# Kernel optimization log

Hardware: AMD Instinct MI355X
Metric: run time of the kernel (lower is better)

## Reference

```python
import jax, jax.numpy as jnp
import numpy as np

B, T, M, PH, PW = 4, 8, 128, 48, 48
QD, CD, H, DH = 1024, 768, 8, 64
INNER = H * DH

def layer_norm(x, g, b, eps=1e-5):
    m = x.mean(-1, keepdims=True)
    v = ((x - m) ** 2).mean(-1, keepdims=True)
    return (x - m) * jax.lax.rsqrt(v + eps) * g + b

def setup_inputs():
    key = jax.random.key(0)
    ks = jax.random.split(key, 10)
    x = jax.random.normal(ks[0], (B * T, PH * PW, QD), jnp.float32)
    context = jax.random.normal(ks[1], (B, M, CD), jnp.float32)
    sg_node_positions = jax.random.normal(ks[2], (B, M, 3), jnp.float32) * 2.0
    # valid c2w: identity rotation + random translation (invertible)
    c2w = jnp.broadcast_to(jnp.eye(4, dtype=jnp.float32), (B, T, 4, 4))
    camera_c2w = c2w.at[..., :3, 3].set(jax.random.normal(ks[3], (B, T, 3), jnp.float32))
    intrinsics = jnp.broadcast_to(jnp.array([[1.0, 0.0, 0.5], [0.0, 1.0, 0.5], [0.0, 0.0, 1.0]], jnp.float32), (B, 3, 3))
    s = 0.02
    Wq = jax.random.normal(ks[4], (QD, INNER), jnp.float32) * s
    Wk = jax.random.normal(ks[5], (CD, INNER), jnp.float32) * s
    Wv = jax.random.normal(ks[6], (CD, INNER), jnp.float32) * s
    Wo = jax.random.normal(ks[7], (INNER, QD), jnp.float32) * s
    gate = jnp.array([0.1], jnp.float32)          # zero-init in module; nonzero so path is active
    spatial_gate = jnp.array([0.1], jnp.float32)
    spatial_log_sigma = jax.random.normal(ks[8], (H,), jnp.float32) * 0.1
    depth_log_alpha = jax.random.normal(ks[9], (H,), jnp.float32) * 0.1
    gamma_q = jnp.ones((QD,), jnp.float32); beta_q = jnp.zeros((QD,), jnp.float32)
    gamma_k = jnp.ones((CD,), jnp.float32); beta_k = jnp.zeros((CD,), jnp.float32)
    return dict(x=x, context=context, sg_node_positions=sg_node_positions, camera_c2w=camera_c2w,
                intrinsics=intrinsics, Wq=Wq, Wk=Wk, Wv=Wv, Wo=Wo, gate=gate, spatial_gate=spatial_gate,
                spatial_log_sigma=spatial_log_sigma, depth_log_alpha=depth_log_alpha,
                gamma_q=gamma_q, beta_q=beta_q, gamma_k=gamma_k, beta_k=beta_k,
                patch_h=PH, patch_w=PW)

def spatial_bias(sg_node_positions, camera_c2w, intrinsics, spatial_log_sigma, depth_log_alpha, patch_h, patch_w):
    Bb, Mn, _ = sg_node_positions.shape
    Tn = camera_c2w.shape[1]
    w2c = jnp.linalg.inv(camera_c2w)
    R = w2c[:, :, :3, :3]
    tv = w2c[:, :, :3, 3]
    p_cam = jnp.einsum('btij,bmj->btmi', R, sg_node_positions) + tv[:, :, None, :]  # (B,T,M,3)
    z = jnp.clip(p_cam[..., 2], 1e-4, None)
    fx = intrinsics[:, 0, 0]; fy = intrinsics[:, 1, 1]
    cx = intrinsics[:, 0, 2]; cy = intrinsics[:, 1, 2]
    u = fx[:, None, None] * (p_cam[..., 0] / z) + cx[:, None, None]   # (B,T,M)
    v = fy[:, None, None] * (p_cam[..., 1] / z) + cy[:, None, None]
    gy = (jnp.arange(patch_h, dtype=jnp.float32) + 0.5) / patch_h
    gx = (jnp.arange(patch_w, dtype=jnp.float32) + 0.5) / patch_w
    gyy, gxx = jnp.meshgrid(gy, gx, indexing='ij')
    gxx = gxx.reshape(-1); gyy = gyy.reshape(-1)                       # (P,)
    sq = (gxx[None, None, :, None] - u[:, :, None, :]) ** 2 + (gyy[None, None, :, None] - v[:, :, None, :]) ** 2  # (B,T,P,M)
    sigma = jnp.exp(spatial_log_sigma)
    inv2s = z[:, :, None, :] ** 2 / (2.0 * sigma[None, None, :, None] ** 2 + 1e-8)  # (B,T,H,M)
    bias = -sq[:, :, None, :, :] * inv2s[:, :, :, None, :]             # (B,T,H,P,M)
    depth_term = depth_log_alpha[None, None, :, None, None] * (-jnp.log(z))[:, :, None, None, :]
    bias = bias + depth_term
    behind = p_cam[..., 2] <= 0.0
    bias = jnp.where(behind[:, :, None, None, :], 0.0, bias)
    return bias.reshape(Bb * Tn, bias.shape[2], patch_h * patch_w, Mn)  # (BT,H,P,M)

def reference(x, context, sg_node_positions, camera_c2w, intrinsics, Wq, Wk, Wv, Wo, gate, spatial_gate,
              spatial_log_sigma, depth_log_alpha, gamma_q, beta_q, gamma_k, beta_k, patch_h, patch_w):
    BT, P, _ = x.shape
    Bb, Mn, _ = context.shape
    Tn = camera_c2w.shape[1]
    q = layer_norm(x, gamma_q, beta_q) @ Wq                            # (BT,P,INNER)
    ck = layer_norm(context, gamma_k, beta_k)
    k = ck @ Wk
    v = ck @ Wv
    q = q.reshape(BT, P, H, DH).transpose(0, 2, 1, 3)                  # (BT,H,P,DH)
    k = jnp.broadcast_to(k.reshape(Bb, 1, Mn, H, DH), (Bb, Tn, Mn, H, DH)).reshape(BT, Mn, H, DH).transpose(0, 2, 1, 3)
    v = jnp.broadcast_to(v.reshape(Bb, 1, Mn, H, DH), (Bb, Tn, Mn, H, DH)).reshape(BT, Mn, H, DH).transpose(0, 2, 1, 3)
    scores = jnp.einsum('bhpd,bhmd->bhpm', q, k) * (DH ** -0.5)        # (BT,H,P,M)
    bias = spatial_bias(sg_node_positions, camera_c2w, intrinsics, spatial_log_sigma, depth_log_alpha, patch_h, patch_w)
    scores = scores + jnp.tanh(spatial_gate) * bias
    attn = jax.nn.softmax(scores, axis=-1)
    out = jnp.einsum('bhpm,bhmd->bhpd', attn, v).transpose(0, 2, 1, 3).reshape(BT, P, INNER)
    return x + jnp.tanh(gate) * (out @ Wo)
```

## Files before the change

kernel.cpp:

```cpp
#include <hip/hip_runtime.h>
#include <hip/hip_bf16.h>
#include <stdint.h>
#include <cstddef>

typedef short short8 __attribute__((ext_vector_type(8)));
typedef float f32x4 __attribute__((ext_vector_type(4)));
typedef unsigned short us4 __attribute__((ext_vector_type(4)));
typedef unsigned short us8 __attribute__((ext_vector_type(8)));

#define DEV static __device__ __forceinline__

DEV unsigned short f2b(float f) {
  __hip_bfloat16 h = __float2bfloat16(f);
  return __builtin_bit_cast(unsigned short, h);
}
DEV float b2f(unsigned short u) {
  unsigned int t = ((unsigned int)u) << 16;
  return __builtin_bit_cast(float, t);
}

DEV void gload_lds16(const void* g, void* lds) {
  __builtin_amdgcn_global_load_lds((const __attribute__((address_space(1))) unsigned int*)g,
                                   (__attribute__((address_space(3))) unsigned int*)lds, 16, 0, 0);
}

__launch_bounds__(512, 2)
__global__ void gemm256_8ph(const unsigned short* __restrict__ A,
                            const unsigned short* __restrict__ Bt,
                            unsigned short* __restrict__ Cb,
                            int M, int N, int K)
{
  __shared__ __attribute__((aligned(16))) char lds[131072];
  const int tid = threadIdx.x;
  const int lane = tid & 63, w = tid >> 6;
  const int wr = w >> 2, wc = w & 3;
  const int g = lane >> 4, lr = lane & 15;
  const int ntile = N >> 8;
  const int nwg = gridDim.x;
  const int bid = blockIdx.x;
  const int tile = ((nwg & 7) == 0) ? ((bid & 7)*(nwg >> 3) + (bid >> 3)) : bid;
  const size_t m0 = (size_t)(tile / ntile) << 8;
  const size_t n0 = (size_t)(tile % ntile) << 8;

  const int srl = tid >> 3;
  const int sgc = ((tid & 7) ^ (srl & 7)) * 8;

#define STAGEH(X, grow0, k0, ldsoff)                                           \
  do {                                                                         \
    char* hb_ = lds + (ldsoff) + w*1024;                                       \
    gload_lds16((X) + ((grow0) + srl)*(size_t)K + (k0) + sgc, hb_);            \
    gload_lds16((X) + ((grow0) + 64 + srl)*(size_t)K + (k0) + sgc, hb_ + 8192);\
  } while (0)

#define BAR() do { __builtin_amdgcn_sched_barrier(0); __builtin_amdgcn_s_barrier(); __builtin_amdgcn_sched_barrier(0); } while (0)

  f32x4 acc[8][4] = {};
  short8 aF[4][2], bF[4][2];

  int aoff[2], boff[2];
#pragma unroll
  for (int kk = 0; kk < 2; ++kk) {
    const int sl = (((kk*4 + g) ^ (lr & 7)) * 16);
    aoff[kk] = wr*16384 + lr*128 + sl;
    boff[kk] = 32768 + (wc >> 1)*16384 + ((wc & 1)*64 + lr)*128 + sl;
  }

#define MFQ(mh, nh)                                                            \
  do {                                                                         \
    __builtin_amdgcn_s_setprio(1);                                             \
    _Pragma("unroll")                                                          \
    for (int kk = 0; kk < 2; ++kk)                                             \
      _Pragma("unroll")                                                        \
      for (int mt = 0; mt < 4; ++mt)                                           \
        _Pragma("unroll")                                                      \
        for (int nt = 0; nt < 2; ++nt)                                         \
          acc[(mh)*4+mt][(nh)*2+nt] = __builtin_amdgcn_mfma_f32_16x16x32_bf16( \
              aF[mt][kk], bF[(nh)*2+nt][kk], acc[(mh)*4+mt][(nh)*2+nt], 0,0,0);\
    __builtin_amdgcn_s_setprio(0);                                             \
  } while (0)

  STAGEH(A,  m0,       0, 0);
  STAGEH(A,  m0 + 128, 0, 16384);
  STAGEH(Bt, n0,       0, 32768);
  STAGEH(Bt, n0 + 128, 0, 49152);
  STAGEH(Bt, n0,       64, 65536 + 32768);
  STAGEH(Bt, n0 + 128, 64, 65536 + 49152);
  asm volatile("s_waitcnt vmcnt(4)" ::: "memory");
  __builtin_amdgcn_s_barrier();

  const int NI = K >> 7;
  for (int i = 0; i < NI; ++i) {
    const int T = 2*i;
    const bool nl = (i + 1 < NI);
    const int kA1 = (T + 1) << 6;
    const int kT2 = (T + 2) << 6;
    const int kT3 = (T + 3) << 6;

#pragma unroll
    for (int kk = 0; kk < 2; ++kk) {
#pragma unroll
      for (int mt = 0; mt < 4; ++mt) aF[mt][kk] = *(const short8*)(lds + mt*2048 + aoff[kk]);
#pragma unroll
      for (int nf = 0; nf < 2; ++nf) bF[nf][kk] = *(const short8*)(lds + nf*2048 + boff[kk]);
    }
    STAGEH(A, m0, kA1, 65536);
    BAR();
    MFQ(0, 0);
    BAR();
#pragma unroll
    for (int kk = 0; kk < 2; ++kk)
#pragma unroll
      for (int nf = 2; nf < 4; ++nf) bF[nf][kk] = *(const short8*)(lds + nf*2048 + boff[kk]);
    STAGEH(A, m0 + 128, kA1, 65536 + 16384);
    BAR();
    MFQ(0, 1);
    BAR();
#pragma unroll
    for (int kk = 0; kk < 2; ++kk)
#pragma unroll
      for (int mt = 0; mt < 4; ++mt) aF[mt][kk] = *(const short8*)(lds + (4+mt)*2048 + aoff[kk]);
    if (nl) STAGEH(Bt, n0, kT2, 32768);
    BAR();
    MFQ(1, 0);
    BAR();
    if (nl) {
      STAGEH(Bt, n0 + 128, kT2, 49152);
      asm volatile("s_waitcnt vmcnt(4)" ::: "memory");
    } else {
      asm volatile("s_waitcnt vmcnt(0)" ::: "memory");
    }
    BAR();
    MFQ(1, 1);
    BAR();

#pragma unroll
    for (int kk = 0; kk < 2; ++kk) {
#pragma unroll
      for (int mt = 0; mt < 4; ++mt) aF[mt][kk] = *(const short8*)(lds + 65536 + mt*2048 + aoff[kk]);
#pragma unroll
      for (int nf = 0; nf < 2; ++nf) bF[nf][kk] = *(const short8*)(lds + 65536 + nf*2048 + boff[kk]);
    }
    if (nl) STAGEH(A, m0, kT2, 0);
    BAR();
    MFQ(0, 0);
    BAR();
#pragma unroll
    for (int kk = 0; kk < 2; ++kk)
#pragma unroll
      for (int nf = 2; nf < 4; ++nf) bF[nf][kk] = *(const short8*)(lds + 65536 + nf*2048 + boff[kk]);
    if (nl) STAGEH(A, m0 + 128, kT2, 16384);
    BAR();
    MFQ(0, 1);
    BAR();
#pragma unroll
    for (int kk = 0; kk < 2; ++kk)
#pragma unroll
      for (int mt = 0; mt < 4; ++mt) aF[mt][kk] = *(const short8*)(lds + 65536 + (4+mt)*2048 + aoff[kk]);
    if (nl) STAGEH(Bt, n0, kT3, 65536 + 32768);
    BAR();
    MFQ(1, 0);
    BAR();
    if (nl) {
      STAGEH(Bt, n0 + 128, kT3, 65536 + 49152);
      asm volatile("s_waitcnt vmcnt(4)" ::: "memory");
    }
    BAR();
    MFQ(1, 1);
    BAR();
  }

  asm volatile("s_waitcnt vmcnt(0)" ::: "memory");
  __builtin_amdgcn_s_barrier();
  float* Sw = (float*)(lds) + w*1024;
#pragma unroll
  for (int mt = 0; mt < 8; ++mt) {
#pragma unroll
    for (int nt = 0; nt < 4; ++nt)
#pragma unroll
      for (int r = 0; r < 4; ++r)
        Sw[(g*4 + r)*64 + nt*16 + lr] = acc[mt][nt][r];
#pragma unroll
    for (int rep = 0; rep < 2; ++rep) {
      const int row2 = rep*8 + (lane >> 3);
      const int colf = (lane & 7)*8;
      f32x4 a0 = *(const f32x4*)(Sw + row2*64 + colf);
      f32x4 a1 = *(const f32x4*)(Sw + row2*64 + colf + 4);
      us8 ov;
#pragma unroll
      for (int j = 0; j < 4; ++j) { ov[j] = f2b(a0[j]); ov[4+j] = f2b(a1[j]); }
      const size_t rowg = m0 + wr*128 + mt*16 + row2;
      *(us8*)(Cb + rowg * (size_t)N + (n0 + wc*64 + colf)) = ov;
    }
  }
#undef STAGEH
#undef BAR
#undef MFQ
}

__launch_bounds__(256, 2)
__global__ void gemm_oproj(const unsigned short* __restrict__ A,
                           const unsigned short* __restrict__ Bt,
                           float* __restrict__ Cf,
                           const unsigned short* __restrict__ lnx,
                           const float* __restrict__ stats,
                           const float* __restrict__ ginv,
                           const float* __restrict__ betaq,
                           const float* __restrict__ gatep,
                           int M, int N, int K)
{
  __shared__ __attribute__((aligned(16))) char As[16384];
  __shared__ __attribute__((aligned(16))) char Bs[16384];
  const int tid  = threadIdx.x;
  const int lane = tid & 63, w = tid >> 6;
  const int wr = w >> 1, wc = w & 1;
  const int g = lane >> 4, lr = lane & 15;
  const int ntile = N >> 7;
  const int nwg = gridDim.x;
  const int bid = blockIdx.x;
  const int tile = ((nwg & 7) == 0) ? ((bid & 7)*(nwg >> 3) + (bid >> 3)) : bid;
  const int m0 = (tile / ntile) << 7;
  const int n0 = (tile % ntile) << 7;

  const int lrow  = lane >> 3;
  const int lslot = (lane & 7) ^ lrow;

  f32x4 acc[4][4] = {};

  for (int k0 = 0; k0 < K; k0 += 64) {
#pragma unroll
    for (int c = 0; c < 4; ++c) {
      const int rowc = (w*4 + c)*8;
      gload_lds16(A  + (size_t)(m0 + rowc + lrow)*K + k0 + lslot*8, As + rowc*128);
      gload_lds16(Bt + (size_t)(n0 + rowc + lrow)*K + k0 + lslot*8, Bs + rowc*128);
    }
    __syncthreads();
#pragma unroll
    for (int ks = 0; ks < 2; ++ks) {
      short8 af[4], bfr[4];
#pragma unroll
      for (int mt = 0; mt < 4; ++mt) {
        int row = wr*64 + mt*16 + lr;
        int slot = (ks*4 + g) ^ (row & 7);
        af[mt] = *(const short8*)(As + row*128 + slot*16);
      }
#pragma unroll
      for (int nt = 0; nt < 4; ++nt) {
        int row = wc*64 + nt*16 + lr;
        int slot = (ks*4 + g) ^ (row & 7);
        bfr[nt] = *(const short8*)(Bs + row*128 + slot*16);
      }
#pragma unroll
      for (int mt = 0; mt < 4; ++mt)
#pragma unroll
        for (int nt = 0; nt < 4; ++nt)
          acc[mt][nt] = __builtin_amdgcn_mfma_f32_16x16x32_bf16(af[mt], bfr[nt], acc[mt][nt], 0, 0, 0);
    }
    __syncthreads();
  }

  float* Sw = (float*)(As) + w*1024;
  const float tg = tanhf(gatep[0]);
#pragma unroll
  for (int mt = 0; mt < 4; ++mt) {
#pragma unroll
    for (int nt = 0; nt < 4; ++nt)
#pragma unroll
      for (int r = 0; r < 4; ++r)
        Sw[(g*4 + r)*64 + nt*16 + lr] = acc[mt][nt][r];
#pragma unroll
    for (int rep = 0; rep < 4; ++rep) {
      const int row2 = rep*4 + g;
      const int colf = lr*4;
      f32x4 val = *(const f32x4*)(Sw + row2*64 + colf);
      const size_t rowg = (size_t)(m0 + wr*64 + mt*16 + row2);
      const size_t col  = (size_t)(n0 + wc*64 + colf);
      const size_t idx  = rowg * (size_t)N + col;
      const float mn = stats[rowg*2 + 0];
      const float sd = stats[rowg*2 + 1];
      us4 lnv = *(const us4*)(lnx + idx);
      f32x4 gi = *(const f32x4*)(ginv + col);
      f32x4 bt4 = *(const f32x4*)(betaq + col);
#pragma unroll
      for (int j = 0; j < 4; ++j) {
        float xr = (b2f(lnv[j]) - bt4[j]) * gi[j] * sd + mn;
        val[j] = xr + tg * val[j];
      }
      *(f32x4*)(Cf + idx) = val;
    }
  }
}

__launch_bounds__(256, 2)
__global__ void gemm_kv(const unsigned short* __restrict__ ck,
                        const unsigned short* __restrict__ Wk_t,
                        const unsigned short* __restrict__ Wv_t,
                        unsigned short* __restrict__ Kb,
                        unsigned short* __restrict__ Vt)
{
  __shared__ __attribute__((aligned(16))) char As[16384];
  __shared__ __attribute__((aligned(16))) char Bs[16384];
  const int bid = blockIdx.x;
  const int kv = bid >> 4, bidl = bid & 15;
  const unsigned short* Bt = kv ? Wv_t : Wk_t;
  const int m0 = (bidl >> 2) << 7, n0 = (bidl & 3) << 7;
  const int tid  = threadIdx.x;
  const int lane = tid & 63, w = tid >> 6;
  const int wr = w >> 1, wc = w & 1;
  const int g = lane >> 4, lr = lane & 15;
  const int lrow  = lane >> 3;
  const int lslot = (lane & 7) ^ lrow;
  const int K = 768;

  f32x4 acc[4][4] = {};

  for (int k0 = 0; k0 < K; k0 += 64) {
#pragma unroll
    for (int c = 0; c < 4; ++c) {
      const int rowc = (w*4 + c)*8;
      gload_lds16(ck + (size_t)(m0 + rowc + lrow)*K + k0 + lslot*8, As + rowc*128);
      gload_lds16(Bt + (size_t)(n0 + rowc + lrow)*K + k0 + lslot*8, Bs + rowc*128);
    }
    __syncthreads();
#pragma unroll
    for (int ks = 0; ks < 2; ++ks) {
      short8 af[4], bfr[4];
#pragma unroll
      for (int mt = 0; mt < 4; ++mt) {
        int row = wr*64 + mt*16 + lr;
        int slot = (ks*4 + g) ^ (row & 7);
        af[mt] = *(const short8*)(As + row*128 + slot*16);
      }
#pragma unroll
      for (int nt = 0; nt < 4; ++nt) {
        int row = wc*64 + nt*16 + lr;
        int slot = (ks*4 + g) ^ (row & 7);
        bfr[nt] = *(const short8*)(Bs + row*128 + slot*16);
      }
#pragma unroll
      for (int mt = 0; mt < 4; ++mt)
#pragma unroll
        for (int nt = 0; nt < 4; ++nt)
          acc[mt][nt] = __builtin_amdgcn_mfma_f32_16x16x32_bf16(af[mt], bfr[nt], acc[mt][nt], 0, 0, 0);
    }
    __syncthreads();
  }

#pragma unroll
  for (int mt = 0; mt < 4; ++mt)
#pragma unroll
    for (int nt = 0; nt < 4; ++nt)
#pragma unroll
      for (int r = 0; r < 4; ++r) {
        int row = m0 + wr*64 + mt*16 + g*4 + r;
        int col = n0 + wc*64 + nt*16 + lr;
        int bb = row >> 7, mm = row & 127, hh = col >> 6, dd = col & 63;
        unsigned short val = f2b(acc[mt][nt][r]);
        if (kv == 0) Kb[(((size_t)(bb*8 + hh))*128 + mm)*64 + dd] = val;
        else         Vt[(((size_t)(bb*8 + hh))*64 + dd)*128 + mm] = val;
      }
}

template<int NSEG>
DEV void ln_rows_body(const float* __restrict__ in, const float* __restrict__ gamma,
                      const float* __restrict__ beta, unsigned short* __restrict__ out,
                      int C, int blk, int tid, float* __restrict__ stats)
{
  const int lane = tid & 63;
  const size_t row = (size_t)blk*4 + (tid >> 6);
  const float* rp = in + row * (size_t)C;
  f32x4 vals[NSEG];
  float s = 0.f, sq = 0.f;
#pragma unroll
  for (int i = 0; i < NSEG; ++i) {
    f32x4 v = *(const f32x4*)(rp + (i*64 + lane)*4);
    vals[i] = v;
#pragma unroll
    for (int j = 0; j < 4; ++j) { s += v[j]; sq += v[j]*v[j]; }
  }
#pragma unroll
  for (int off = 32; off >= 1; off >>= 1) {
    s  += __shfl_xor(s, off);
    sq += __shfl_xor(sq, off);
  }
  const float invC = 1.0f / (float)C;
  float mean = s * invC;
  float var  = sq * invC - mean*mean;
  float rstd = rsqrtf(var + 1e-5f);
  if (stats && lane == 0) {
    stats[row*2 + 0] = mean;
    stats[row*2 + 1] = 1.0f / rstd;
  }
#pragma unroll
  for (int i = 0; i < NSEG; ++i) {
    int cb = (i*64 + lane)*4;
    f32x4 gm = *(const f32x4*)(gamma + cb);
    f32x4 bb = *(const f32x4*)(beta + cb);
    us4 ov;
#pragma unroll
    for (int j = 0; j < 4; ++j)
      ov[j] = f2b((vals[i][j] - mean)*rstd*gm[j] + bb[j]);
    *(us4*)(out + row * (size_t)C + cb) = ov;
  }
}

__global__ void prep(const float* __restrict__ x, const float* __restrict__ gq,
                     const float* __restrict__ bq, unsigned short* __restrict__ ln_x,
                     float* __restrict__ stats, float* __restrict__ ginv,
                     const float* __restrict__ Wq, const float* __restrict__ Wk,
                     const float* __restrict__ Wv, const float* __restrict__ Wo,
                     unsigned short* __restrict__ Wq_t, unsigned short* __restrict__ Wk_t,
                     unsigned short* __restrict__ Wv_t, unsigned short* __restrict__ Wo_t,
                     const float* __restrict__ ctx, const float* __restrict__ gk,
                     const float* __restrict__ bk, unsigned short* __restrict__ ck,
                     const float* __restrict__ pos, const float* __restrict__ c2w,
                     const float* __restrict__ intr, const float* __restrict__ sls,
                     const float* __restrict__ dla,
                     float* __restrict__ u_o, float* __restrict__ v_o, float* __restrict__ bh_o,
                     float* __restrict__ iv_o, float* __restrict__ dp_o)
{
  __shared__ float tile[32][33];
  int bidx = blockIdx.x;
  if (bidx < 18432) {
    ln_rows_body<4>(x, gq, bq, ln_x, 1024, bidx, threadIdx.x, stats);
    return;
  }
  bidx -= 18432;
  if (bidx < 1792) {
    const float* src; unsigned short* dst; int R, C;
    if (bidx < 512)       { src = Wq; dst = Wq_t; R = 1024; C = 512; }
    else if (bidx < 896)  { src = Wk; dst = Wk_t; R = 768;  C = 512;  bidx -= 512; }
    else if (bidx < 1280) { src = Wv; dst = Wv_t; R = 768;  C = 512;  bidx -= 896; }
    else                  { src = Wo; dst = Wo_t; R = 512;  C = 1024; bidx -= 1280; }
    const int cb = C >> 5;
    const int bx = bidx % cb, by = bidx / cb;
    const int tx = threadIdx.x & 31, ty = threadIdx.x >> 5;
#pragma unroll
    for (int i = 0; i < 32; i += 8)
      tile[ty + i][tx] = src[(size_t)(by*32 + ty + i)*C + bx*32 + tx];
    __syncthreads();
#pragma unroll
    for (int i = 0; i < 32; i += 8)
      dst[(size_t)(bx*32 + ty + i)*R + by*32 + tx] = f2b(tile[tx][ty + i]);
    return;
  }
  bidx -= 1792;
  if (bidx < 128) {
    ln_rows_body<3>(ctx, gk, bk, ck, 768, bidx, threadIdx.x, nullptr);
    return;
  }
  bidx -= 128;
  if (bidx < 32) {
    if (threadIdx.x >= 128) return;
    const int bt = bidx;
    const int b = bt >> 3;
    const int m = threadIdx.x;
    const float* Mc = c2w + (size_t)bt*16;
    float r00=Mc[0], r01=Mc[1], r02=Mc[2],  t0=Mc[3];
    float r10=Mc[4], r11=Mc[5], r12=Mc[6],  t1=Mc[7];
    float r20=Mc[8], r21=Mc[9], r22=Mc[10], t2=Mc[11];
    float a00 = r11*r22 - r12*r21;
    float a01 = r02*r21 - r01*r22;
    float a02 = r01*r12 - r02*r11;
    float a10 = r12*r20 - r10*r22;
    float a11 = r00*r22 - r02*r20;
    float a12 = r02*r10 - r00*r12;
    float a20 = r10*r21 - r11*r20;
    float a21 = r01*r20 - r00*r21;
    float a22 = r00*r11 - r01*r10;
    float det = r00*a00 + r01*a10 + r02*a20;
    float id = 1.0f/det;
    a00*=id; a01*=id; a02*=id; a10*=id; a11*=id; a12*=id; a20*=id; a21*=id; a22*=id;
    float tv0 = -(a00*t0 + a01*t1 + a02*t2);
    float tv1 = -(a10*t0 + a11*t1 + a12*t2);
    float tv2 = -(a20*t0 + a21*t1 + a22*t2);
    const float* pm = pos + (size_t)(b*128 + m)*3;
    float px = pm[0], py = pm[1], pz = pm[2];
    float xx = a00*px + a01*py + a02*pz + tv0;
    float yy = a10*px + a11*py + a12*pz + tv1;
    float zraw = a20*px + a21*py + a22*pz + tv2;
    float z = fmaxf(zraw, 1e-4f);
    float fx = intr[b*9 + 0], fy = intr[b*9 + 4], cx = intr[b*9 + 2], cy = intr[b*9 + 5];
    u_o[bt*128 + m] = fx*(xx/z) + cx;
    v_o[bt*128 + m] = fy*(yy/z) + cy;
    bh_o[bt*128 + m] = (zraw <= 0.0f) ? 1.0f : 0.0f;
    float lz = __logf(z);
#pragma unroll
    for (int hh = 0; hh < 8; ++hh) {
      float sg = __expf(sls[hh]);
      iv_o[(size_t)(bt*8 + hh)*128 + m] = z*z / (2.0f*sg*sg + 1e-8f);
      dp_o[(size_t)(bt*8 + hh)*128 + m] = dla[hh] * (-lz);
    }
    return;
  }
#pragma unroll
  for (int i = 0; i < 4; ++i) {
    int c = i*256 + threadIdx.x;
    ginv[c] = 1.0f / gq[c];
  }
}

__launch_bounds__(256, 2)
__global__ void attn_kernel(const unsigned short* __restrict__ q,
                            const unsigned short* __restrict__ Kb,
                            const unsigned short* __restrict__ Vt,
                            const float* __restrict__ ub, const float* __restrict__ vb,
                            const float* __restrict__ bhb,
                            const float* __restrict__ ivb, const float* __restrict__ dpb,
                            const float* __restrict__ sgate,
                            unsigned short* __restrict__ out)
{
  const int bid = blockIdx.x;
  const int ptile = bid % 18;
  const int h  = (bid / 18) & 7;
  const int bt = bid / (18*8);
  const int b  = bt >> 3;
  const int lane = threadIdx.x & 63, w = threadIdx.x >> 6;
  const int g = lane >> 4, lr = lane & 15;
  const int p0 = ptile*128 + w*32;

  const float sg = tanhf(sgate[0]);
  const unsigned short* Kh = Kb + ((size_t)(b*8 + h)) * (128*64);
  const unsigned short* Vh = Vt + ((size_t)(b*8 + h)) * (64*128);
  const unsigned short* qh = q + (size_t)bt*2304*512 + h*64;

  short8 qf[2][2];
#pragma unroll
  for (int pt = 0; pt < 2; ++pt)
#pragma unroll
    for (int ks = 0; ks < 2; ++ks)
      qf[pt][ks] = *(const short8*)(qh + (size_t)(p0 + pt*16 + lr)*512 + ks*32 + g*8);

  f32x4 st[8][2] = {};
#pragma unroll
  for (int mt = 0; mt < 8; ++mt) {
#pragma unroll
    for (int ks = 0; ks < 2; ++ks) {
      short8 kf = *(const short8*)(Kh + (mt*16 + lr)*64 + ks*32 + g*8);
#pragma unroll
      for (int pt = 0; pt < 2; ++pt)
        st[mt][pt] = __builtin_amdgcn_mfma_f32_16x16x32_bf16(kf, qf[pt][ks], st[mt][pt], 0, 0, 0);
    }
  }

  float gx[2], gy[2];
#pragma unroll
  for (int pt = 0; pt < 2; ++pt) {
    int p = p0 + pt*16 + lr;
    int py = p / 48, px = p - py*48;
    gx[pt] = (px + 0.5f) * (1.0f/48.0f);
    gy[pt] = (py + 0.5f) * (1.0f/48.0f);
  }
  const float* uB = ub  + bt*128;
  const float* vB = vb  + bt*128;
  const float* bB = bhb + bt*128;
  const float* iB = ivb + (size_t)(bt*8 + h)*128;
  const float* dB = dpb + (size_t)(bt*8 + h)*128;

  float pmax[2] = {-3.0e38f, -3.0e38f};
#pragma unroll
  for (int mt = 0; mt < 8; ++mt) {
    int mb = mt*16 + g*4;
    f32x4 uu = *(const f32x4*)(uB + mb);
    f32x4 vv = *(const f32x4*)(vB + mb);
    f32x4 bh = *(const f32x4*)(bB + mb);
    f32x4 iv = *(const f32x4*)(iB + mb);
    f32x4 dp = *(const f32x4*)(dB + mb);
#pragma unroll
    for (int r = 0; r < 4; ++r) {
#pragma unroll
      for (int pt = 0; pt < 2; ++pt) {
        float du = gx[pt] - uu[r], dv = gy[pt] - vv[r];
        float bias = (bh[r] != 0.0f) ? 0.0f : (-(du*du + dv*dv)*iv[r] + dp[r]);
        float s = st[mt][pt][r]*0.125f + sg*bias;
        st[mt][pt][r] = s;
        pmax[pt] = fmaxf(pmax[pt], s);
      }
    }
  }
#pragma unroll
  for (int pt = 0; pt < 2; ++pt) {
    pmax[pt] = fmaxf(pmax[pt], __shfl_xor(pmax[pt], 16));
    pmax[pt] = fmaxf(pmax[pt], __shfl_xor(pmax[pt], 32));
  }
  float psum[2] = {0.f, 0.f};
#pragma unroll
  for (int mt = 0; mt < 8; ++mt)
#pragma unroll
    for (int pt = 0; pt < 2; ++pt)
#pragma unroll
      for (int r = 0; r < 4; ++r) {
        float e = __expf(st[mt][pt][r] - pmax[pt]);
        st[mt][pt][r] = e;
        psum[pt] += e;
      }
#pragma unroll
  for (int pt = 0; pt < 2; ++pt) {
    psum[pt] += __shfl_xor(psum[pt], 16);
    psum[pt] += __shfl_xor(psum[pt], 32);
  }
  float pinv[2] = {1.0f/psum[0], 1.0f/psum[1]};

  short8 pf[2][4];
#pragma unroll
  for (int pt = 0; pt < 2; ++pt)
#pragma unroll
    for (int ms = 0; ms < 4; ++ms)
#pragma unroll
      for (int i = 0; i < 8; ++i)
        pf[pt][ms][i] = (short)f2b(st[ms*2 + (i>>2)][pt][i & 3] * pinv[pt]);

  f32x4 o[4][2] = {};
#pragma unroll
  for (int ms = 0; ms < 4; ++ms) {
#pragma unroll
    for (int dt = 0; dt < 4; ++dt) {
      const unsigned short* vp = Vh + (size_t)(dt*16 + lr)*128 + ms*32 + g*4;
      us4 v0 = *(const us4*)(vp);
      us4 v1 = *(const us4*)(vp + 16);
      short8 vf;
#pragma unroll
      for (int i = 0; i < 4; ++i) { vf[i] = (short)v0[i]; vf[i+4] = (short)v1[i]; }
#pragma unroll
      for (int pt = 0; pt < 2; ++pt)
        o[dt][pt] = __builtin_amdgcn_mfma_f32_16x16x32_bf16(vf, pf[pt][ms], o[dt][pt], 0, 0, 0);
    }
  }

#pragma unroll
  for (int dt = 0; dt < 4; ++dt)
#pragma unroll
    for (int pt = 0; pt < 2; ++pt) {
      int p = p0 + pt*16 + lr;
      int d = h*64 + dt*16 + g*4;
      us4 ov;
#pragma unroll
      for (int r = 0; r < 4; ++r) ov[r] = f2b(o[dt][pt][r]);
      *(us4*)(out + (size_t)(bt*2304 + p)*512 + d) = ov;
    }
}

extern "C" void kernel_launch(void* const* d_in, const int* in_sizes, int n_in,
                              void* d_out, int out_size, void* d_ws, size_t ws_size,
                              hipStream_t stream)
{
  const float* x     = (const float*)d_in[0];
  const float* ctx   = (const float*)d_in[1];
  const float* pos   = (const float*)d_in[2];
  const float* c2w   = (const float*)d_in[3];
  const float* intr  = (const float*)d_in[4];
  const float* Wq    = (const float*)d_in[5];
  const float* Wk    = (const float*)d_in[6];
  const float* Wv    = (const float*)d_in[7];
  const float* Wo    = (const float*)d_in[8];
  const float* gate  = (const float*)d_in[9];
  const float* sgate = (const float*)d_in[10];
  const float* sls   = (const float*)d_in[11];
  const float* dla   = (const float*)d_in[12];
  const float* gq    = (const float*)d_in[13];
  const float* bq    = (const float*)d_in[14];
  const float* gk    = (const float*)d_in[15];
  const float* bk    = (const float*)d_in[16];

  char* ws = (char*)d_ws;
  size_t off = 0;
  auto alloc = [&](size_t bytes) {
    char* p = ws + off;
    off += (bytes + 255) & ~(size_t)255;
    return p;
  };
  unsigned short* ln_x     = (unsigned short*)alloc(73728ull*1024*2);
  unsigned short* attn_out = (unsigned short*)alloc(73728ull*512*2);
  unsigned short* qbuf     = (unsigned short*)alloc(73728ull*512*2);
  float*          stats    = (float*)alloc(73728ull*2*4);
  float*          ginv     = (float*)alloc(1024*4);
  unsigned short* Wq_t  = (unsigned short*)alloc(512ull*1024*2);
  unsigned short* Wk_t  = (unsigned short*)alloc(512ull*768*2);
  unsigned short* Wv_t  = (unsigned short*)alloc(512ull*768*2);
  unsigned short* Wo_t  = (unsigned short*)alloc(1024ull*512*2);
  unsigned short* ck    = (unsigned short*)alloc(512ull*768*2);
  unsigned short* Kbuf  = (unsigned short*)alloc(4ull*8*128*64*2);
  unsigned short* Vtb   = (unsigned short*)alloc(4ull*8*64*128*2);
  float* u_o  = (float*)alloc(32*128*4);
  float* v_o  = (float*)alloc(32*128*4);
  float* bh_o = (float*)alloc(32*128*4);
  float* iv_o = (float*)alloc(32ull*8*128*4);
  float* dp_o = (float*)alloc(32ull*8*128*4);

  prep<<<20385, 256, 0, stream>>>(x, gq, bq, ln_x, stats, ginv,
                                  Wq, Wk, Wv, Wo, Wq_t, Wk_t, Wv_t, Wo_t,
                                  ctx, gk, bk, ck,
                                  pos, c2w, intr, sls, dla,
                                  u_o, v_o, bh_o, iv_o, dp_o);

  gemm_kv<<<32, 256, 0, stream>>>(ck, Wk_t, Wv_t, Kbuf, Vtb);

  gemm256_8ph<<<(73728/256)*(512/256), 512, 0, stream>>>(ln_x, Wq_t, qbuf, 73728, 512, 1024);

  attn_kernel<<<32*8*18, 256, 0, stream>>>(qbuf, Kbuf, Vtb, u_o, v_o, bh_o, iv_o, dp_o, sgate, attn_out);

  gemm_oproj<<<(73728/128)*(1024/128), 256, 0, stream>>>(attn_out, Wo_t, (float*)d_out,
                                                         ln_x, stats, ginv, bq, gate,
                                                         73728, 1024, 512);
}
```

Baseline: 501.1 us.

## Fuse Q projection GEMM with attention, keeping Q tiles in LDS

```diff
diff --git a/kernel.cpp b/kernel.cpp
--- a/kernel.cpp
+++ b/kernel.cpp
@@ -25,22 +25,27 @@
 }
 
 __launch_bounds__(512, 2)
-__global__ void gemm256_8ph(const unsigned short* __restrict__ A,
-                            const unsigned short* __restrict__ Bt,
-                            unsigned short* __restrict__ Cb,
-                            int M, int N, int K)
+__global__ void qattn(const unsigned short* __restrict__ A,
+                      const unsigned short* __restrict__ Bt,
+                      const unsigned short* __restrict__ Kb,
+                      const unsigned short* __restrict__ Vt,
+                      const float* __restrict__ ub, const float* __restrict__ vb,
+                      const float* __restrict__ bhb,
+                      const float* __restrict__ ivb, const float* __restrict__ dpb,
+                      const float* __restrict__ sgate,
+                      unsigned short* __restrict__ out)
 {
   __shared__ __attribute__((aligned(16))) char lds[131072];
+  const int K = 1024;
   const int tid = threadIdx.x;
   const int lane = tid & 63, w = tid >> 6;
   const int wr = w >> 2, wc = w & 3;
   const int g = lane >> 4, lr = lane & 15;
-  const int ntile = N >> 8;
   const int nwg = gridDim.x;
   const int bid = blockIdx.x;
-  const int tile = ((nwg & 7) == 0) ? ((bid & 7)*(nwg >> 3) + (bid >> 3)) : bid;
-  const size_t m0 = (size_t)(tile / ntile) << 8;
-  const size_t n0 = (size_t)(tile % ntile) << 8;
+  const int tile = (bid & 7)*(nwg >> 3) + (bid >> 3);
+  const size_t m0 = (size_t)(tile >> 1) << 8;
+  const int n0 = (tile & 1) << 8;
 
   const int srl = tid >> 3;
   const int sgc = ((tid & 7) ^ (srl & 7)) * 8;
@@ -171,26 +176,149 @@
 
   asm volatile("s_waitcnt vmcnt(0)" ::: "memory");
   __builtin_amdgcn_s_barrier();
-  float* Sw = (float*)(lds) + w*1024;
-#pragma unroll
-  for (int mt = 0; mt < 8; ++mt) {
+  char* qlds = lds + w*16384;
+#pragma unroll
+  for (int mt = 0; mt < 8; ++mt)
 #pragma unroll
     for (int nt = 0; nt < 4; ++nt)
 #pragma unroll
-      for (int r = 0; r < 4; ++r)
-        Sw[(g*4 + r)*64 + nt*16 + lr] = acc[mt][nt][r];
-#pragma unroll
-    for (int rep = 0; rep < 2; ++rep) {
-      const int row2 = rep*8 + (lane >> 3);
-      const int colf = (lane & 7)*8;
-      f32x4 a0 = *(const f32x4*)(Sw + row2*64 + colf);
-      f32x4 a1 = *(const f32x4*)(Sw + row2*64 + colf + 4);
-      us8 ov;
-#pragma unroll
-      for (int j = 0; j < 4; ++j) { ov[j] = f2b(a0[j]); ov[4+j] = f2b(a1[j]); }
-      const size_t rowg = m0 + wr*128 + mt*16 + row2;
-      *(us8*)(Cb + rowg * (size_t)N + (n0 + wc*64 + colf)) = ov;
-    }
+      for (int r = 0; r < 4; ++r) {
+        const int row = mt*16 + g*4 + r;
+        const int d   = nt*16 + lr;
+        const int byte = row*128 + (((d >> 3) ^ (row & 7))*16) + (d & 7)*2;
+        *(unsigned short*)(qlds + byte) = f2b(acc[mt][nt][r]);
+      }
+  asm volatile("s_waitcnt lgkmcnt(0)" ::: "memory");
+  __builtin_amdgcn_sched_barrier(0);
+
+  const int h  = (n0 >> 6) + wc;
+  const int bt = (int)(m0 / 2304);
+  const int b  = bt >> 3;
+  const int prow0 = (int)(m0 % 2304) + wr*128;
+  const float sg = tanhf(sgate[0]);
+  const unsigned short* Kh = Kb + ((size_t)(b*8 + h)) * (128*64);
+  const unsigned short* Vh = Vt + ((size_t)(b*8 + h)) * (64*128);
+  const float* uB = ub  + bt*128;
+  const float* vB = vb  + bt*128;
+  const float* bB = bhb + bt*128;
+  const float* iB = ivb + (size_t)(bt*8 + h)*128;
+  const float* dB = dpb + (size_t)(bt*8 + h)*128;
+
+  for (int pc = 0; pc < 4; ++pc) {
+    const int p0 = prow0 + pc*32;
+
+    short8 qf[2][2];
+#pragma unroll
+    for (int pt = 0; pt < 2; ++pt)
+#pragma unroll
+      for (int ks = 0; ks < 2; ++ks) {
+        const int row = pc*32 + pt*16 + lr;
+        const int slot = (ks*4 + g) ^ (row & 7);
+        qf[pt][ks] = *(const short8*)(qlds + row*128 + slot*16);
+      }
+
+    f32x4 st[8][2] = {};
+#pragma unroll
+    for (int mt = 0; mt < 8; ++mt) {
+#pragma unroll
+      for (int ks = 0; ks < 2; ++ks) {
+        short8 kf = *(const short8*)(Kh + (mt*16 + lr)*64 + ks*32 + g*8);
+#pragma unroll
+        for (int pt = 0; pt < 2; ++pt)
+          st[mt][pt] = __builtin_amdgcn_mfma_f32_16x16x32_bf16(kf, qf[pt][ks], st[mt][pt], 0, 0, 0);
+      }
+    }
+
+    float gx[2], gy[2];
+#pragma unroll
+    for (int pt = 0; pt < 2; ++pt) {
+      int p = p0 + pt*16 + lr;
+      int py = p / 48, px = p - py*48;
+      gx[pt] = (px + 0.5f) * (1.0f/48.0f);
+      gy[pt] = (py + 0.5f) * (1.0f/48.0f);
+    }
+
+    float pmax[2] = {-3.0e38f, -3.0e38f};
+#pragma unroll
+    for (int mt = 0; mt < 8; ++mt) {
+      int mb = mt*16 + g*4;
+      f32x4 uu = *(const f32x4*)(uB + mb);
+      f32x4 vv = *(const f32x4*)(vB + mb);
+      f32x4 bh = *(const f32x4*)(bB + mb);
+      f32x4 iv = *(const f32x4*)(iB + mb);
+      f32x4 dp = *(const f32x4*)(dB + mb);
+#pragma unroll
+      for (int r = 0; r < 4; ++r) {
+#pragma unroll
+        for (int pt = 0; pt < 2; ++pt) {
+          float du = gx[pt] - uu[r], dv = gy[pt] - vv[r];
+          float bias = (bh[r] != 0.0f) ? 0.0f : (-(du*du + dv*dv)*iv[r] + dp[r]);
+          float s = st[mt][pt][r]*0.125f + sg*bias;
+          st[mt][pt][r] = s;
+          pmax[pt] = fmaxf(pmax[pt], s);
+        }
+      }
+    }
+#pragma unroll
+    for (int pt = 0; pt < 2; ++pt) {
+      pmax[pt] = fmaxf(pmax[pt], __shfl_xor(pmax[pt], 16));
+      pmax[pt] = fmaxf(pmax[pt], __shfl_xor(pmax[pt], 32));
+    }
+    float psum[2] = {0.f, 0.f};
+#pragma unroll
+    for (int mt = 0; mt < 8; ++mt)
+#pragma unroll
+      for (int pt = 0; pt < 2; ++pt)
+#pragma unroll
+        for (int r = 0; r < 4; ++r) {
+          float e = __expf(st[mt][pt][r] - pmax[pt]);
+          st[mt][pt][r] = e;
+          psum[pt] += e;
+        }
+#pragma unroll
+    for (int pt = 0; pt < 2; ++pt) {
+      psum[pt] += __shfl_xor(psum[pt], 16);
+      psum[pt] += __shfl_xor(psum[pt], 32);
+    }
+    float pinv[2] = {1.0f/psum[0], 1.0f/psum[1]};
+
+    short8 pf[2][4];
+#pragma unroll
+    for (int pt = 0; pt < 2; ++pt)
+#pragma unroll
+      for (int ms = 0; ms < 4; ++ms)
+#pragma unroll
+        for (int i = 0; i < 8; ++i)
+          pf[pt][ms][i] = (short)f2b(st[ms*2 + (i>>2)][pt][i & 3] * pinv[pt]);
+
+    f32x4 o[4][2] = {};
+#pragma unroll
+    for (int ms = 0; ms < 4; ++ms) {
+#pragma unroll
+      for (int dt = 0; dt < 4; ++dt) {
+        const unsigned short* vp = Vh + (size_t)(dt*16 + lr)*128 + ms*32 + g*4;
+        us4 v0 = *(const us4*)(vp);
+        us4 v1 = *(const us4*)(vp + 16);
+        short8 vf;
+#pragma unroll
+        for (int i = 0; i < 4; ++i) { vf[i] = (short)v0[i]; vf[i+4] = (short)v1[i]; }
+#pragma unroll
+        for (int pt = 0; pt < 2; ++pt)
+          o[dt][pt] = __builtin_amdgcn_mfma_f32_16x16x32_bf16(vf, pf[pt][ms], o[dt][pt], 0, 0, 0);
+      }
+    }
+
+#pragma unroll
+    for (int dt = 0; dt < 4; ++dt)
+#pragma unroll
+      for (int pt = 0; pt < 2; ++pt) {
+        const int p = p0 + pt*16 + lr;
+        const int d = h*64 + dt*16 + g*4;
+        us4 ov;
+#pragma unroll
+        for (int r = 0; r < 4; ++r) ov[r] = f2b(o[dt][pt][r]);
+        *(us4*)(out + (size_t)(bt*2304 + p)*512 + d) = ov;
+      }
   }
 #undef STAGEH
 #undef BAR
@@ -499,146 +627,6 @@
   }
 }
 
-__launch_bounds__(256, 2)
-__global__ void attn_kernel(const unsigned short* __restrict__ q,
-                            const unsigned short* __restrict__ Kb,
-                            const unsigned short* __restrict__ Vt,
-                            const float* __restrict__ ub, const float* __restrict__ vb,
-                            const float* __restrict__ bhb,
-                            const float* __restrict__ ivb, const float* __restrict__ dpb,
-                            const float* __restrict__ sgate,
-                            unsigned short* __restrict__ out)
-{
-  const int bid = blockIdx.x;
-  const int ptile = bid % 18;
-  const int h  = (bid / 18) & 7;
-  const int bt = bid / (18*8);
-  const int b  = bt >> 3;
-  const int lane = threadIdx.x & 63, w = threadIdx.x >> 6;
-  const int g = lane >> 4, lr = lane & 15;
-  const int p0 = ptile*128 + w*32;
-
-  const float sg = tanhf(sgate[0]);
-  const unsigned short* Kh = Kb + ((size_t)(b*8 + h)) * (128*64);
-  const unsigned short* Vh = Vt + ((size_t)(b*8 + h)) * (64*128);
-  const unsigned short* qh = q + (size_t)bt*2304*512 + h*64;
-
-  short8 qf[2][2];
-#pragma unroll
-  for (int pt = 0; pt < 2; ++pt)
-#pragma unroll
-    for (int ks = 0; ks < 2; ++ks)
-      qf[pt][ks] = *(const short8*)(qh + (size_t)(p0 + pt*16 + lr)*512 + ks*32 + g*8);
-
-  f32x4 st[8][2] = {};
-#pragma unroll
-  for (int mt = 0; mt < 8; ++mt) {
-#pragma unroll
-    for (int ks = 0; ks < 2; ++ks) {
-      short8 kf = *(const short8*)(Kh + (mt*16 + lr)*64 + ks*32 + g*8);
-#pragma unroll
-      for (int pt = 0; pt < 2; ++pt)
-        st[mt][pt] = __builtin_amdgcn_mfma_f32_16x16x32_bf16(kf, qf[pt][ks], st[mt][pt], 0, 0, 0);
-    }
-  }
-
-  float gx[2], gy[2];
-#pragma unroll
-  for (int pt = 0; pt < 2; ++pt) {
-    int p = p0 + pt*16 + lr;
-    int py = p / 48, px = p - py*48;
-    gx[pt] = (px + 0.5f) * (1.0f/48.0f);
-    gy[pt] = (py + 0.5f) * (1.0f/48.0f);
-  }
-  const float* uB = ub  + bt*128;
-  const float* vB = vb  + bt*128;
-  const float* bB = bhb + bt*128;
-  const float* iB = ivb + (size_t)(bt*8 + h)*128;
-  const float* dB = dpb + (size_t)(bt*8 + h)*128;
-
-  float pmax[2] = {-3.0e38f, -3.0e38f};
-#pragma unroll
-  for (int mt = 0; mt < 8; ++mt) {
-    int mb = mt*16 + g*4;
-    f32x4 uu = *(const f32x4*)(uB + mb);
-    f32x4 vv = *(const f32x4*)(vB + mb);
-    f32x4 bh = *(const f32x4*)(bB + mb);
-    f32x4 iv = *(const f32x4*)(iB + mb);
-    f32x4 dp = *(const f32x4*)(dB + mb);
-#pragma unroll
-    for (int r = 0; r < 4; ++r) {
-#pragma unroll
-      for (int pt = 0; pt < 2; ++pt) {
-        float du = gx[pt] - uu[r], dv = gy[pt] - vv[r];
-        float bias = (bh[r] != 0.0f) ? 0.0f : (-(du*du + dv*dv)*iv[r] + dp[r]);
-        float s = st[mt][pt][r]*0.125f + sg*bias;
-        st[mt][pt][r] = s;
-        pmax[pt] = fmaxf(pmax[pt], s);
-      }
-    }
-  }
-#pragma unroll
-  for (int pt = 0; pt < 2; ++pt) {
-    pmax[pt] = fmaxf(pmax[pt], __shfl_xor(pmax[pt], 16));
-    pmax[pt] = fmaxf(pmax[pt], __shfl_xor(pmax[pt], 32));
-  }
-  float psum[2] = {0.f, 0.f};
-#pragma unroll
-  for (int mt = 0; mt < 8; ++mt)
-#pragma unroll
-    for (int pt = 0; pt < 2; ++pt)
-#pragma unroll
-      for (int r = 0; r < 4; ++r) {
-        float e = __expf(st[mt][pt][r] - pmax[pt]);
-        st[mt][pt][r] = e;
-        psum[pt] += e;
-      }
-#pragma unroll
-  for (int pt = 0; pt < 2; ++pt) {
-    psum[pt] += __shfl_xor(psum[pt], 16);
-    psum[pt] += __shfl_xor(psum[pt], 32);
-  }
-  float pinv[2] = {1.0f/psum[0], 1.0f/psum[1]};
-
-  short8 pf[2][4];
-#pragma unroll
-  for (int pt = 0; pt < 2; ++pt)
-#pragma unroll
-    for (int ms = 0; ms < 4; ++ms)
-#pragma unroll
-      for (int i = 0; i < 8; ++i)
-        pf[pt][ms][i] = (short)f2b(st[ms*2 + (i>>2)][pt][i & 3] * pinv[pt]);
-
-  f32x4 o[4][2] = {};
-#pragma unroll
-  for (int ms = 0; ms < 4; ++ms) {
-#pragma unroll
-    for (int dt = 0; dt < 4; ++dt) {
-      const unsigned short* vp = Vh + (size_t)(dt*16 + lr)*128 + ms*32 + g*4;
-      us4 v0 = *(const us4*)(vp);
-      us4 v1 = *(const us4*)(vp + 16);
-      short8 vf;
-#pragma unroll
-      for (int i = 0; i < 4; ++i) { vf[i] = (short)v0[i]; vf[i+4] = (short)v1[i]; }
-#pragma unroll
-      for (int pt = 0; pt < 2; ++pt)
-        o[dt][pt] = __builtin_amdgcn_mfma_f32_16x16x32_bf16(vf, pf[pt][ms], o[dt][pt], 0, 0, 0);
-    }
-  }
-
-#pragma unroll
-  for (int dt = 0; dt < 4; ++dt)
-#pragma unroll
-    for (int pt = 0; pt < 2; ++pt) {
-      int p = p0 + pt*16 + lr;
-      int d = h*64 + dt*16 + g*4;
-      us4 ov;
-#pragma unroll
-      for (int r = 0; r < 4; ++r) ov[r] = f2b(o[dt][pt][r]);
-      *(us4*)(out + (size_t)(bt*2304 + p)*512 + d) = ov;
-    }
-}
-
 extern "C" void kernel_launch(void* const* d_in, const int* in_sizes, int n_in,
                               void* d_out, int out_size, void* d_ws, size_t ws_size,
                               hipStream_t stream)
@@ -670,7 +658,6 @@
   };
   unsigned short* ln_x     = (unsigned short*)alloc(73728ull*1024*2);
   unsigned short* attn_out = (unsigned short*)alloc(73728ull*512*2);
-  unsigned short* qbuf     = (unsigned short*)alloc(73728ull*512*2);
   float*          stats    = (float*)alloc(73728ull*2*4);
   float*          ginv     = (float*)alloc(1024*4);
   unsigned short* Wq_t  = (unsigned short*)alloc(512ull*1024*2);
@@ -694,9 +681,8 @@
 
   gemm_kv<<<32, 256, 0, stream>>>(ck, Wk_t, Wv_t, Kbuf, Vtb);
 
-  gemm256_8ph<<<(73728/256)*(512/256), 512, 0, stream>>>(ln_x, Wq_t, qbuf, 73728, 512, 1024);
-
-  attn_kernel<<<32*8*18, 256, 0, stream>>>(qbuf, Kbuf, Vtb, u_o, v_o, bh_o, iv_o, dp_o, sgate, attn_out);
+  qattn<<<576, 512, 0, stream>>>(ln_x, Wq_t, Kbuf, Vtb,
+                                 u_o, v_o, bh_o, iv_o, dp_o, sgate, attn_out);
 
   gemm_oproj<<<(73728/128)*(1024/128), 256, 0, stream>>>(attn_out, Wo_t, (float*)d_out,
                                                          ln_x, stats, ginv, bq, gate,
```

Result: no change. 509.8 us (+1.7%).
